# Kernel tuning notes

Measured on AMD Instinct MI355X. Metric: run time of the kernel, lower is better.

Reference implementation:

```python
import jax, jax.numpy as jnp
import numpy as np

N_NODES = 100000
N_EDGES = 1600000
FEAT = 128
HID = 128
CLS = 4


def setup_inputs() -> dict:
    key = jax.random.key(0)
    ks = jax.random.split(key, 10)
    x = jax.random.normal(ks[0], (N_NODES, FEAT), dtype=jnp.float32)
    edge_index = jax.random.randint(ks[1], (2, N_EDGES), 0, N_NODES, dtype=jnp.int64)
    s1 = 1.0 / np.sqrt(FEAT)
    s2 = 1.0 / np.sqrt(HID)
    s3 = 1.0 / np.sqrt(CLS)
    return {
        "x": x,
        "edge_index": edge_index,
        "W1l": jax.random.uniform(ks[2], (HID, FEAT), jnp.float32, -s1, s1),
        "b1": jax.random.uniform(ks[3], (HID,), jnp.float32, -s1, s1),
        "W1r": jax.random.uniform(ks[4], (HID, FEAT), jnp.float32, -s1, s1),
        "W2l": jax.random.uniform(ks[5], (CLS, HID), jnp.float32, -s2, s2),
        "b2": jax.random.uniform(ks[6], (CLS,), jnp.float32, -s2, s2),
        "W2r": jax.random.uniform(ks[7], (CLS, HID), jnp.float32, -s2, s2),
        "Wlin": jax.random.uniform(ks[8], (2, CLS), jnp.float32, -s3, s3),
        "blin": jax.random.uniform(ks[9], (2,), jnp.float32, -s3, s3),
    }


def _sage_conv(h, src, dst, Wl, bl, Wr, n_nodes):
    # PyG SAGEConv (mean aggr, root_weight=True): lin_l(mean_j h_j) + lin_r(h_i)
    msg = h[src]  # [E, d] irregular gather
    agg = jax.ops.segment_sum(msg, dst, num_segments=n_nodes)  # [N, d]
    deg = jax.ops.segment_sum(jnp.ones((src.shape[0], 1), h.dtype), dst,
                              num_segments=n_nodes)  # [N, 1]
    agg = agg / jnp.maximum(deg, 1.0)
    return agg @ Wl.T + bl + h @ Wr.T


def reference(x, edge_index, W1l, b1, W1r, W2l, b2, W2r, Wlin, blin):
    n = x.shape[0]
    src, dst = edge_index[0], edge_index[1]
    h = jax.nn.relu(_sage_conv(x, src, dst, W1l, b1, W1r, n))
    # dropout is identity in eval mode (training=False)
    h = _sage_conv(h, src, dst, W2l, b2, W2r, n)  # [N, 4]
    return h @ Wlin.T + blin  # [N, 2]
```

## Files before the change

### kernel.cpp

```cpp
#include <hip/hip_runtime.h>

#define NN 100000
#define NE 1600000
#define NBUK 1563
#define EB 8192

typedef __attribute__((ext_vector_type(8))) short v8s;
typedef __attribute__((ext_vector_type(4))) float v4f;

__device__ __forceinline__ unsigned short f2bf(float f) {
  unsigned int u = __float_as_uint(f);
  unsigned int r = (u + 0x7FFFu + ((u >> 16) & 1u)) >> 16;
  return (unsigned short)r;
}
__device__ __forceinline__ float bflo(unsigned int w) { return __uint_as_float(w << 16); }
__device__ __forceinline__ float bfhi(unsigned int w) { return __uint_as_float(w & 0xFFFF0000u); }
__device__ __forceinline__ float bf2f(unsigned short w) {
  return __uint_as_float((unsigned int)w << 16);
}


__global__ void k_zerob(int* __restrict__ hist) {
  int i = blockIdx.x * blockDim.x + threadIdx.x;
  if (i < NBUK) hist[i] = 0;
}

__global__ __launch_bounds__(256) void k_hist(const int* __restrict__ dst,
                                              int* __restrict__ hist) {
  __shared__ int lh[NBUK];
  int t = threadIdx.x;
  for (int i = t; i < NBUK; i += 256) lh[i] = 0;
  __syncthreads();
  int base = blockIdx.x * 4096;
  int lim = min(4096, NE - base);
  for (int j = t; j < lim; j += 256) atomicAdd(&lh[dst[base + j] >> 6], 1);
  __syncthreads();
  for (int i = t; i < NBUK; i += 256) {
    int c = lh[i];
    if (c) atomicAdd(&hist[i], c);
  }
}

__global__ __launch_bounds__(256) void k_scanb(const int* __restrict__ hist,
                                               int* __restrict__ bbase,
                                               int* __restrict__ gcur) {
  __shared__ int wsum[4];
  int t = threadIdx.x, w = t >> 6, l = t & 63;
  int carry = 0;
  for (int c = 0; c < (NBUK + 255) / 256; ++c) {
    int i = c * 256 + t;
    int vv = (i < NBUK) ? hist[i] : 0;
    int inc = vv;
#pragma unroll
    for (int o = 1; o < 64; o <<= 1) {
      int uu = __shfl_up(inc, o, 64);
      if (l >= o) inc += uu;
    }
    if (l == 63) wsum[w] = inc;
    __syncthreads();
    int woff = 0;
    for (int j = 0; j < w; ++j) woff += wsum[j];
    int excl = carry + woff + inc - vv;
    if (i < NBUK) { bbase[i] = excl; gcur[i] = excl; }
    int tot = wsum[0] + wsum[1] + wsum[2] + wsum[3];
    __syncthreads();
    carry += tot;
  }
}

__global__ __launch_bounds__(256) void k_scatter(const int* __restrict__ src,
                                                 const int* __restrict__ dst,
                                                 int* __restrict__ gcur,
                                                 unsigned int* __restrict__ staged) {
  __shared__ int lhist[NBUK];
  __shared__ int lcur[NBUK];
  __shared__ int gclaim[NBUK];
  int t = threadIdx.x;
  int e0 = blockIdx.x * EB;
  int ecnt = min(EB, NE - e0);
  for (int i = t; i < NBUK; i += 256) { lhist[i] = 0; lcur[i] = 0; }
  __syncthreads();
  for (int j = t; j < ecnt; j += 256) atomicAdd(&lhist[dst[e0 + j] >> 6], 1);
  __syncthreads();
  for (int b = t; b < NBUK; b += 256) {
    int c = lhist[b];
    gclaim[b] = c ? atomicAdd(&gcur[b], c) : 0;
  }
  __syncthreads();
  for (int j = t; j < ecnt; j += 256) {
    int s = src[e0 + j], d = dst[e0 + j];
    int b = d >> 6;
    int lp = atomicAdd(&lcur[b], 1);
    staged[gclaim[b] + lp] = ((unsigned int)s << 6) | (unsigned int)(d & 63);
  }
}

__global__ __launch_bounds__(256) void k_sort2(const unsigned int* __restrict__ staged,
                                               const int* __restrict__ bbase,
                                               const int* __restrict__ hist,
                                               int* __restrict__ csr,
                                               int* __restrict__ off,
                                               int* __restrict__ deg) {
  __shared__ int h64[64], c64[64];
  int bkt = blockIdx.x, t = threadIdx.x;
  if (t < 64) h64[t] = 0;
  __syncthreads();
  int st = bbase[bkt], cnt = hist[bkt];
  for (int j = t; j < cnt; j += 256) atomicAdd(&h64[staged[st + j] & 63], 1);
  __syncthreads();
  if (t < 64) {
    int v = h64[t];
    int inc = v;
    for (int o = 1; o < 64; o <<= 1) {
      int uu = __shfl_up(inc, o, 64);
      if (t >= o) inc += uu;
    }
    int excl = inc - v;
    c64[t] = excl;
    int node = bkt * 64 + t;
    if (node < NN) { off[node] = st + excl; deg[node] = v; }
  }
  __syncthreads();
  for (int j = t; j < cnt; j += 256) {
    unsigned pk = staged[st + j];
    int lp = atomicAdd(&c64[pk & 63], 1);
    csr[st + lp] = (int)(pk >> 6);
  }
}

extern __shared__ char smem_dyn[];
__global__ __launch_bounds__(512) void k_gemm1(
    const float* __restrict__ x, const float* __restrict__ W1l,
    const float* __restrict__ W1r,
    unsigned short* __restrict__ u, unsigned short* __restrict__ v) {
  char* wlds = smem_dyn;
  int t = threadIdx.x;
  {
    int rsub = t >> 4, chunk = t & 15;
#pragma unroll
    for (int rd = 0; rd < 8; ++rd) {
      int row = rd * 32 + rsub;
      const float* wsrc = (row < 128) ? (W1l + (size_t)row * 128 + chunk * 8)
                                      : (W1r + (size_t)(row - 128) * 128 + chunk * 8);
      float4 f0 = *(const float4*)wsrc;
      float4 f1 = *(const float4*)(wsrc + 4);
      unsigned d0 = (unsigned)f2bf(f0.x) | ((unsigned)f2bf(f0.y) << 16);
      unsigned d1 = (unsigned)f2bf(f0.z) | ((unsigned)f2bf(f0.w) << 16);
      unsigned d2 = (unsigned)f2bf(f1.x) | ((unsigned)f2bf(f1.y) << 16);
      unsigned d3 = (unsigned)f2bf(f1.z) | ((unsigned)f2bf(f1.w) << 16);
      *(uint4*)(wlds + row * 272 + chunk * 16) = make_uint4(d0, d1, d2, d3);
    }
  }

  int wave = t >> 6, l = t & 63;
  int m0 = blockIdx.x * 128 + wave * 16;
  int lr = l & 15, kq = l >> 4;
  int rowc = min(m0 + lr, NN - 1);

  v8s a[4];
#pragma unroll
  for (int ks = 0; ks < 4; ++ks) {
    const float* xp = x + (size_t)rowc * 128 + ks * 32 + kq * 8;
    float4 f0 = *(const float4*)xp;
    float4 f1 = *(const float4*)(xp + 4);
    v8s tv;
    tv[0] = (short)f2bf(f0.x); tv[1] = (short)f2bf(f0.y);
    tv[2] = (short)f2bf(f0.z); tv[3] = (short)f2bf(f0.w);
    tv[4] = (short)f2bf(f1.x); tv[5] = (short)f2bf(f1.y);
    tv[6] = (short)f2bf(f1.z); tv[7] = (short)f2bf(f1.w);
    a[ks] = tv;
  }

  __syncthreads();

  v4f acc[16];
#pragma unroll
  for (int nt = 0; nt < 16; ++nt) acc[nt] = (v4f){0.f, 0.f, 0.f, 0.f};

#pragma unroll
  for (int nt = 0; nt < 16; ++nt) {
    const char* wrow = wlds + (nt * 16 + lr) * 272;
#pragma unroll
    for (int ks = 0; ks < 4; ++ks) {
      v8s b = *(const v8s*)(wrow + ks * 64 + kq * 16);
      acc[nt] = __builtin_amdgcn_mfma_f32_16x16x32_bf16(b, a[ks], acc[nt], 0, 0, 0);
    }
  }

  if (m0 + lr < NN) {
    size_t rowb = (size_t)(m0 + lr) * 128;
#pragma unroll
    for (int nt = 0; nt < 16; ++nt) {
      unsigned lo = (unsigned)f2bf(acc[nt][0]) | ((unsigned)f2bf(acc[nt][1]) << 16);
      unsigned hi = (unsigned)f2bf(acc[nt][2]) | ((unsigned)f2bf(acc[nt][3]) << 16);
      int col = (nt & 7) * 16 + kq * 4;
      if (nt < 8) *(uint2*)(u + rowb + col) = make_uint2(lo, hi);
      else        *(uint2*)(v + rowb + col) = make_uint2(lo, hi);
    }
  }
}

__global__ __launch_bounds__(256) void k_agg(
    const unsigned short* __restrict__ u, const unsigned short* __restrict__ v,
    const int* __restrict__ csr, const int* __restrict__ off, const int* __restrict__ deg,
    const float* __restrict__ b1,
    const float* __restrict__ W2l, const float* __restrict__ W2r,
    float* __restrict__ p, float* __restrict__ r) {
  int wid = (blockIdx.x * blockDim.x + threadIdx.x) >> 6;
  int l = threadIdx.x & 63;
  if (wid >= NN) return;
  int cnt = deg[wid], st = off[wid];
  int half = l >> 5;
  int dpos = l & 31;
  const char* ubase = (const char*)u + (dpos << 3);

  uint2 vw = *(const uint2*)((const char*)v + ((size_t)wid << 8) + (dpos << 3));
  float4 bb = *(const float4*)(b1 + 4 * dpos);
  const float* Wbase = half ? W2r : W2l;
  float4 wv[4];
#pragma unroll
  for (int o = 0; o < 4; ++o) wv[o] = *(const float4*)(Wbase + o * 128 + 4 * dpos);

  float a0 = 0.f, a1 = 0.f, a2 = 0.f, a3 = 0.f;

#define LOADW(W, S) uint2 W = *(const uint2*)(ubase + ((size_t)((unsigned)(S) << 8)))
#define ACCW(W) { a0 += bflo(W.x); a1 += bfhi(W.x); a2 += bflo(W.y); a3 += bfhi(W.y); }

  for (int base = 0; base < cnt; base += 64) {
    int nloc = min(64, cnt - base);
    int idx = 0;
    if (l < nloc) idx = csr[st + base + l];
    int npair = nloc >> 1;
    int e = 0;
    for (; e + 8 <= npair; e += 8) {
      int s0 = __shfl(idx, 2 * e + half, 64);
      int s1 = __shfl(idx, 2 * (e + 1) + half, 64);
      int s2 = __shfl(idx, 2 * (e + 2) + half, 64);
      int s3 = __shfl(idx, 2 * (e + 3) + half, 64);
      int s4 = __shfl(idx, 2 * (e + 4) + half, 64);
      int s5 = __shfl(idx, 2 * (e + 5) + half, 64);
      int s6 = __shfl(idx, 2 * (e + 6) + half, 64);
      int s7 = __shfl(idx, 2 * (e + 7) + half, 64);
      LOADW(w0, s0);
      LOADW(w1, s1);
      LOADW(w2, s2);
      LOADW(w3, s3);
      LOADW(w4, s4);
      LOADW(w5, s5);
      LOADW(w6, s6);
      LOADW(w7, s7);
      ACCW(w0); ACCW(w1); ACCW(w2); ACCW(w3);
      ACCW(w4); ACCW(w5); ACCW(w6); ACCW(w7);
    }
    for (; e + 4 <= npair; e += 4) {
      int s0 = __shfl(idx, 2 * e + half, 64);
      int s1 = __shfl(idx, 2 * (e + 1) + half, 64);
      int s2 = __shfl(idx, 2 * (e + 2) + half, 64);
      int s3 = __shfl(idx, 2 * (e + 3) + half, 64);
      LOADW(w0, s0);
      LOADW(w1, s1);
      LOADW(w2, s2);
      LOADW(w3, s3);
      ACCW(w0); ACCW(w1); ACCW(w2); ACCW(w3);
    }
    for (; e < npair; ++e) {
      int s = __shfl(idx, 2 * e + half, 64);
      LOADW(w, s);
      ACCW(w);
    }
    if (nloc & 1) {
      int s = __shfl(idx, nloc - 1, 64);
      if (half == 0) {
        LOADW(w, s);
        ACCW(w);
      }
    }
  }
#undef LOADW
#undef ACCW

  a0 += __shfl_xor(a0, 32, 64);
  a1 += __shfl_xor(a1, 32, 64);
  a2 += __shfl_xor(a2, 32, 64);
  a3 += __shfl_xor(a3, 32, 64);

  float inv = 1.f / (float)max(cnt, 1);
  float h0 = fmaxf(fmaf(a0, inv, bflo(vw.x) + bb.x), 0.f);
  float h1 = fmaxf(fmaf(a1, inv, bfhi(vw.x) + bb.y), 0.f);
  float h2 = fmaxf(fmaf(a2, inv, bflo(vw.y) + bb.z), 0.f);
  float h3 = fmaxf(fmaf(a3, inv, bfhi(vw.y) + bb.w), 0.f);

  float t0 = h0 * wv[0].x + h1 * wv[0].y + h2 * wv[0].z + h3 * wv[0].w;
  float t1 = h0 * wv[1].x + h1 * wv[1].y + h2 * wv[1].z + h3 * wv[1].w;
  float t2 = h0 * wv[2].x + h1 * wv[2].y + h2 * wv[2].z + h3 * wv[2].w;
  float t3 = h0 * wv[3].x + h1 * wv[3].y + h2 * wv[3].z + h3 * wv[3].w;
  float v01 = (l & 1) ? t1 : t0;
  float w01 = __shfl_xor((l & 1) ? t0 : t1, 1, 64);
  float r01 = v01 + w01;
  float v23 = (l & 1) ? t3 : t2;
  float w23 = __shfl_xor((l & 1) ? t2 : t3, 1, 64);
  float r23 = v23 + w23;
  float vq = (l & 2) ? r23 : r01;
  float wq = __shfl_xor((l & 2) ? r01 : r23, 2, 64);
  float rr = vq + wq;
  rr += __shfl_xor(rr, 4, 64);
  rr += __shfl_xor(rr, 8, 64);
  rr += __shfl_xor(rr, 16, 64);
  float* outp = half ? r : p;
  if (dpos < 4) outp[(size_t)wid * 4 + dpos] = rr;
}

__global__ __launch_bounds__(256) void k_final(
    const float* __restrict__ p, const float* __restrict__ r,
    const int* __restrict__ csr, const int* __restrict__ off,
    const int* __restrict__ deg,
    const float* __restrict__ b2,
    const float* __restrict__ Wlin, const float* __restrict__ blin,
    float* __restrict__ out) {
  int gid = blockIdx.x * blockDim.x + threadIdx.x;
  int node = gid >> 3;
  int sl = gid & 7;
  if (node >= NN) return;
  int cnt = deg[node], st = off[node];
  int l = threadIdx.x & 63;

  float a0 = 0.f, a1 = 0.f, a2 = 0.f, a3 = 0.f;
  for (int e = sl; e < cnt; e += 8) {
    int s = csr[st + e];
    const float4 pv = *(const float4*)(p + (size_t)s * 4);
    a0 += pv.x; a1 += pv.y; a2 += pv.z; a3 += pv.w;
  }
  float v01 = (l & 1) ? a1 : a0;
  float w01 = __shfl_xor((l & 1) ? a0 : a1, 1, 64);
  float r01 = v01 + w01;
  float v23 = (l & 1) ? a3 : a2;
  float w23 = __shfl_xor((l & 1) ? a2 : a3, 1, 64);
  float r23 = v23 + w23;
  float vq = (l & 2) ? r23 : r01;
  float wq = __shfl_xor((l & 2) ? r01 : r23, 2, 64);
  float rr = vq + wq;
  rr += __shfl_xor(rr, 4, 64);
  int o = sl & 3;
  float inv = 1.f / (float)max(cnt, 1);
  float g = rr * inv + b2[o] + r[(size_t)node * 4 + o];
  float t0 = g * Wlin[o];
  float t1 = g * Wlin[4 + o];
  float vv = (l & 1) ? t1 : t0;
  float ww = __shfl_xor((l & 1) ? t0 : t1, 1, 64);
  float q = vv + ww;
  q += __shfl_xor(q, 2, 64);
  if (sl < 2) out[(size_t)node * 2 + sl] = q + blin[sl];
}


extern "C" void kernel_launch(void* const* d_in, const int* in_sizes, int n_in,
                              void* d_out, int out_size, void* d_ws, size_t ws_size,
                              hipStream_t stream) {
  const float* x    = (const float*)d_in[0];
  const int*   ei   = (const int*)d_in[1];
  const int*   src  = ei;
  const int*   dst  = ei + NE;
  const float* W1l  = (const float*)d_in[2];
  const float* b1   = (const float*)d_in[3];
  const float* W1r  = (const float*)d_in[4];
  const float* W2l  = (const float*)d_in[5];
  const float* b2   = (const float*)d_in[6];
  const float* W2r  = (const float*)d_in[7];
  const float* Wlin = (const float*)d_in[8];
  const float* blin = (const float*)d_in[9];
  float* out = (float*)d_out;

  char* w = (char*)d_ws;
  size_t o = 0;
  auto alloc = [&](size_t bytes) {
    void* pp = (void*)(w + o);
    o = (o + bytes + 255) & ~(size_t)255;
    return pp;
  };
  int* hist  = (int*)alloc(NBUK * 4);
  int* bbase = (int*)alloc(NBUK * 4);
  int* gcur  = (int*)alloc(NBUK * 4);
  unsigned int*  staged = (unsigned int*)alloc((size_t)NE * 4);
  int* csr   = (int*)alloc((size_t)NE * 4);
  int* offs  = (int*)alloc(NN * 4);
  int* deg   = (int*)alloc(NN * 4);
  unsigned short* ubuf  = (unsigned short*)alloc((size_t)NN * 128 * 2);
  unsigned short* vbuf  = (unsigned short*)alloc((size_t)NN * 128 * 2);
  float* pbuf = (float*)alloc((size_t)NN * 4 * 4);
  float* rbuf = (float*)alloc((size_t)NN * 4 * 4);

  const size_t gemm1_lds = 256 * 272;

  hipLaunchKernelGGL(k_zerob, dim3((NBUK + 255) / 256), dim3(256), 0, stream, hist);
  hipLaunchKernelGGL(k_hist,  dim3((NE + 4095) / 4096), dim3(256), 0, stream, dst, hist);
  hipLaunchKernelGGL(k_scanb, dim3(1), dim3(256), 0, stream, hist, bbase, gcur);
  hipLaunchKernelGGL(k_scatter, dim3((NE + EB - 1) / EB), dim3(256), 0, stream,
                     src, dst, gcur, staged);
  hipLaunchKernelGGL(k_sort2, dim3(NBUK), dim3(256), 0, stream,
                     staged, bbase, hist, csr, offs, deg);
  hipLaunchKernelGGL(k_gemm1, dim3((NN + 127) / 128), dim3(512), gemm1_lds, stream,
                     x, W1l, W1r, ubuf, vbuf);
  hipLaunchKernelGGL(k_agg,   dim3((NN * 64 + 255) / 256), dim3(256), 0, stream,
                     ubuf, vbuf, csr, offs, deg, b1, W2l, W2r, pbuf, rbuf);
  hipLaunchKernelGGL(k_final, dim3((NN * 8 + 255) / 256), dim3(256), 0, stream,
                     pbuf, rbuf, csr, offs, deg, b2, Wlin, blin, out);
}
```

Measured before the change: 269.2 us.

## Replace bucketed two-pass CSR sort with global atomic degree count and fill

Drops the bucket histogram, scatter and per-bucket local-sort kernels used to build the CSR. It now counts per-node degree with global atomics, runs a three-kernel exclusive scan, and fills the CSR by atomically claiming slots per destination. This avoids the staged intermediate buffer and its extra pass, but brings heavy global atomic contention and a nondeterministic neighbor order inside each row. The aggregation kernel is also split into two half-node launches.

```diff
diff --git a/kernel.cpp b/kernel.cpp
--- a/kernel.cpp
+++ b/kernel.cpp
@@ -2,8 +2,7 @@
 
 #define NN 100000
 #define NE 1600000
-#define NBUK 1563
-#define EB 8192
+#define NHALF 50000
 
 typedef __attribute__((ext_vector_type(8))) short v8s;
 typedef __attribute__((ext_vector_type(4))) float v4f;
@@ -15,41 +14,42 @@
 }
 __device__ __forceinline__ float bflo(unsigned int w) { return __uint_as_float(w << 16); }
 __device__ __forceinline__ float bfhi(unsigned int w) { return __uint_as_float(w & 0xFFFF0000u); }
-__device__ __forceinline__ float bf2f(unsigned short w) {
-  return __uint_as_float((unsigned int)w << 16);
-}
-
-
-__global__ void k_zerob(int* __restrict__ hist) {
+
+
+__global__ __launch_bounds__(256) void k_deg(const int* __restrict__ dst,
+                                             int* __restrict__ deg) {
   int i = blockIdx.x * blockDim.x + threadIdx.x;
-  if (i < NBUK) hist[i] = 0;
-}
-
-__global__ __launch_bounds__(256) void k_hist(const int* __restrict__ dst,
-                                              int* __restrict__ hist) {
-  __shared__ int lh[NBUK];
-  int t = threadIdx.x;
-  for (int i = t; i < NBUK; i += 256) lh[i] = 0;
+  if (i < NE) atomicAdd(&deg[dst[i]], 1);
+}
+
+__global__ __launch_bounds__(256) void k_scan1(const int* __restrict__ deg,
+                                               int* __restrict__ off,
+                                               int* __restrict__ bsum) {
+  __shared__ int wsum[4];
+  int t = threadIdx.x, w = t >> 6, l = t & 63;
+  int i = blockIdx.x * 256 + t;
+  int vv = (i < NN) ? deg[i] : 0;
+  int inc = vv;
+#pragma unroll
+  for (int o = 1; o < 64; o <<= 1) {
+    int uu = __shfl_up(inc, o, 64);
+    if (l >= o) inc += uu;
+  }
+  if (l == 63) wsum[w] = inc;
   __syncthreads();
-  int base = blockIdx.x * 4096;
-  int lim = min(4096, NE - base);
-  for (int j = t; j < lim; j += 256) atomicAdd(&lh[dst[base + j] >> 6], 1);
-  __syncthreads();
-  for (int i = t; i < NBUK; i += 256) {
-    int c = lh[i];
-    if (c) atomicAdd(&hist[i], c);
-  }
-}
-
-__global__ __launch_bounds__(256) void k_scanb(const int* __restrict__ hist,
-                                               int* __restrict__ bbase,
-                                               int* __restrict__ gcur) {
+  int woff = 0;
+  for (int j = 0; j < w; ++j) woff += wsum[j];
+  if (i < NN) off[i] = woff + inc - vv;
+  if (t == 255) bsum[blockIdx.x] = woff + inc;
+}
+
+__global__ __launch_bounds__(256) void k_scan2(int* __restrict__ bsum, int nb) {
   __shared__ int wsum[4];
   int t = threadIdx.x, w = t >> 6, l = t & 63;
   int carry = 0;
-  for (int c = 0; c < (NBUK + 255) / 256; ++c) {
+  for (int c = 0; c * 256 < nb; ++c) {
     int i = c * 256 + t;
-    int vv = (i < NBUK) ? hist[i] : 0;
+    int vv = (i < nb) ? bsum[i] : 0;
     int inc = vv;
 #pragma unroll
     for (int o = 1; o < 64; o <<= 1) {
@@ -60,71 +60,32 @@
     __syncthreads();
     int woff = 0;
     for (int j = 0; j < w; ++j) woff += wsum[j];
-    int excl = carry + woff + inc - vv;
-    if (i < NBUK) { bbase[i] = excl; gcur[i] = excl; }
+    if (i < nb) bsum[i] = carry + woff + inc - vv;
     int tot = wsum[0] + wsum[1] + wsum[2] + wsum[3];
     __syncthreads();
     carry += tot;
   }
 }
 
-__global__ __launch_bounds__(256) void k_scatter(const int* __restrict__ src,
-                                                 const int* __restrict__ dst,
-                                                 int* __restrict__ gcur,
-                                                 unsigned int* __restrict__ staged) {
-  __shared__ int lhist[NBUK];
-  __shared__ int lcur[NBUK];
-  __shared__ int gclaim[NBUK];
-  int t = threadIdx.x;
-  int e0 = blockIdx.x * EB;
-  int ecnt = min(EB, NE - e0);
-  for (int i = t; i < NBUK; i += 256) { lhist[i] = 0; lcur[i] = 0; }
-  __syncthreads();
-  for (int j = t; j < ecnt; j += 256) atomicAdd(&lhist[dst[e0 + j] >> 6], 1);
-  __syncthreads();
-  for (int b = t; b < NBUK; b += 256) {
-    int c = lhist[b];
-    gclaim[b] = c ? atomicAdd(&gcur[b], c) : 0;
-  }
-  __syncthreads();
-  for (int j = t; j < ecnt; j += 256) {
-    int s = src[e0 + j], d = dst[e0 + j];
-    int b = d >> 6;
-    int lp = atomicAdd(&lcur[b], 1);
-    staged[gclaim[b] + lp] = ((unsigned int)s << 6) | (unsigned int)(d & 63);
-  }
-}
-
-__global__ __launch_bounds__(256) void k_sort2(const unsigned int* __restrict__ staged,
-                                               const int* __restrict__ bbase,
-                                               const int* __restrict__ hist,
-                                               int* __restrict__ csr,
+__global__ __launch_bounds__(256) void k_scan3(const int* __restrict__ bsum,
                                                int* __restrict__ off,
-                                               int* __restrict__ deg) {
-  __shared__ int h64[64], c64[64];
-  int bkt = blockIdx.x, t = threadIdx.x;
-  if (t < 64) h64[t] = 0;
-  __syncthreads();
-  int st = bbase[bkt], cnt = hist[bkt];
-  for (int j = t; j < cnt; j += 256) atomicAdd(&h64[staged[st + j] & 63], 1);
-  __syncthreads();
-  if (t < 64) {
-    int v = h64[t];
-    int inc = v;
-    for (int o = 1; o < 64; o <<= 1) {
-      int uu = __shfl_up(inc, o, 64);
-      if (t >= o) inc += uu;
-    }
-    int excl = inc - v;
-    c64[t] = excl;
-    int node = bkt * 64 + t;
-    if (node < NN) { off[node] = st + excl; deg[node] = v; }
-  }
-  __syncthreads();
-  for (int j = t; j < cnt; j += 256) {
-    unsigned pk = staged[st + j];
-    int lp = atomicAdd(&c64[pk & 63], 1);
-    csr[st + lp] = (int)(pk >> 6);
+                                               int* __restrict__ gcur) {
+  int i = blockIdx.x * 256 + threadIdx.x;
+  if (i < NN) {
+    int o = off[i] + bsum[blockIdx.x];
+    off[i] = o;
+    gcur[i] = o;
+  }
+}
+
+__global__ __launch_bounds__(256) void k_fill(const int* __restrict__ src,
+                                              const int* __restrict__ dst,
+                                              int* __restrict__ gcur,
+                                              int* __restrict__ csr) {
+  int i = blockIdx.x * blockDim.x + threadIdx.x;
+  if (i < NE) {
+    int pos = atomicAdd(&gcur[dst[i]], 1);
+    csr[pos] = src[i];
   }
 }
 
@@ -205,8 +166,8 @@
     const int* __restrict__ csr, const int* __restrict__ off, const int* __restrict__ deg,
     const float* __restrict__ b1,
     const float* __restrict__ W2l, const float* __restrict__ W2r,
-    float* __restrict__ p, float* __restrict__ r) {
-  int wid = (blockIdx.x * blockDim.x + threadIdx.x) >> 6;
+    float* __restrict__ p, float* __restrict__ r, int nbase) {
+  int wid = nbase + ((blockIdx.x * blockDim.x + threadIdx.x) >> 6);
   int l = threadIdx.x & 63;
   if (wid >= NN) return;
   int cnt = deg[wid], st = off[wid];
@@ -377,31 +338,32 @@
     o = (o + bytes + 255) & ~(size_t)255;
     return pp;
   };
-  int* hist  = (int*)alloc(NBUK * 4);
-  int* bbase = (int*)alloc(NBUK * 4);
-  int* gcur  = (int*)alloc(NBUK * 4);
-  unsigned int*  staged = (unsigned int*)alloc((size_t)NE * 4);
+  int* deg   = (int*)alloc(NN * 4);
+  int* offs  = (int*)alloc(NN * 4);
+  int* gcur  = (int*)alloc(NN * 4);
+  int* bsum  = (int*)alloc(512 * 4);
   int* csr   = (int*)alloc((size_t)NE * 4);
-  int* offs  = (int*)alloc(NN * 4);
-  int* deg   = (int*)alloc(NN * 4);
   unsigned short* ubuf  = (unsigned short*)alloc((size_t)NN * 128 * 2);
   unsigned short* vbuf  = (unsigned short*)alloc((size_t)NN * 128 * 2);
   float* pbuf = (float*)alloc((size_t)NN * 4 * 4);
   float* rbuf = (float*)alloc((size_t)NN * 4 * 4);
 
+  const int NB = (NN + 255) / 256;
   const size_t gemm1_lds = 256 * 272;
 
-  hipLaunchKernelGGL(k_zerob, dim3((NBUK + 255) / 256), dim3(256), 0, stream, hist);
-  hipLaunchKernelGGL(k_hist,  dim3((NE + 4095) / 4096), dim3(256), 0, stream, dst, hist);
-  hipLaunchKernelGGL(k_scanb, dim3(1), dim3(256), 0, stream, hist, bbase, gcur);
-  hipLaunchKernelGGL(k_scatter, dim3((NE + EB - 1) / EB), dim3(256), 0, stream,
-                     src, dst, gcur, staged);
-  hipLaunchKernelGGL(k_sort2, dim3(NBUK), dim3(256), 0, stream,
-                     staged, bbase, hist, csr, offs, deg);
+  hipMemsetAsync(deg, 0, (size_t)NN * 4, stream);
+  hipLaunchKernelGGL(k_deg,   dim3((NE + 255) / 256), dim3(256), 0, stream, dst, deg);
+  hipLaunchKernelGGL(k_scan1, dim3(NB), dim3(256), 0, stream, deg, offs, bsum);
+  hipLaunchKernelGGL(k_scan2, dim3(1), dim3(256), 0, stream, bsum, NB);
+  hipLaunchKernelGGL(k_scan3, dim3(NB), dim3(256), 0, stream, bsum, offs, gcur);
+  hipLaunchKernelGGL(k_fill,  dim3((NE + 255) / 256), dim3(256), 0, stream,
+                     src, dst, gcur, csr);
   hipLaunchKernelGGL(k_gemm1, dim3((NN + 127) / 128), dim3(512), gemm1_lds, stream,
                      x, W1l, W1r, ubuf, vbuf);
-  hipLaunchKernelGGL(k_agg,   dim3((NN * 64 + 255) / 256), dim3(256), 0, stream,
-                     ubuf, vbuf, csr, offs, deg, b1, W2l, W2r, pbuf, rbuf);
+  hipLaunchKernelGGL(k_agg,   dim3(NHALF * 64 / 256), dim3(256), 0, stream,
+                     ubuf, vbuf, csr, offs, deg, b1, W2l, W2r, pbuf, rbuf, 0);
+  hipLaunchKernelGGL(k_agg,   dim3(NHALF * 64 / 256), dim3(256), 0, stream,
+                     ubuf, vbuf, csr, offs, deg, b1, W2l, W2r, pbuf, rbuf, NHALF);
   hipLaunchKernelGGL(k_final, dim3((NN * 8 + 255) / 256), dim3(256), 0, stream,
                      pbuf, rbuf, csr, offs, deg, b2, Wlin, blin, out);
 }
```

New measurement: 404.8 us. 1.5x slower.

## Fuse CSR build kernels into one cooperative kernel with grid syncs

Applied to the files above, without the earlier changes.

Replaces five separate preprocessing launches (zero, histogram, scan, scatter, per-bucket sort) with a single cooperative kernel of 512 blocks that uses grid.sync between phases. The per-block local histogram is kept in LDS and reused for the scatter claim, so dst is no longer re-histogrammed. The aim is to remove kernel launch gaps and one extra pass over dst. In exchange the scan runs on one block while the others wait at a grid barrier, each block handles about 3125 edges and loops over several buckets in the sort phase, and a cooperative launch is required.

```diff
diff --git a/kernel.cpp b/kernel.cpp
--- a/kernel.cpp
+++ b/kernel.cpp
@@ -1,9 +1,13 @@
 #include <hip/hip_runtime.h>
+#include <hip/hip_cooperative_groups.h>
+
+namespace cg = cooperative_groups;
 
 #define NN 100000
 #define NE 1600000
 #define NBUK 1563
-#define EB 8192
+#define PREB 512
+#define EPB (NE / PREB)
 
 typedef __attribute__((ext_vector_type(8))) short v8s;
 typedef __attribute__((ext_vector_type(4))) float v4f;
@@ -15,116 +19,101 @@
 }
 __device__ __forceinline__ float bflo(unsigned int w) { return __uint_as_float(w << 16); }
 __device__ __forceinline__ float bfhi(unsigned int w) { return __uint_as_float(w & 0xFFFF0000u); }
-__device__ __forceinline__ float bf2f(unsigned short w) {
-  return __uint_as_float((unsigned int)w << 16);
-}
-
-
-__global__ void k_zerob(int* __restrict__ hist) {
-  int i = blockIdx.x * blockDim.x + threadIdx.x;
-  if (i < NBUK) hist[i] = 0;
-}
-
-__global__ __launch_bounds__(256) void k_hist(const int* __restrict__ dst,
-                                              int* __restrict__ hist) {
+
+__global__ __launch_bounds__(256) void k_pre(
+    const int* __restrict__ src, const int* __restrict__ dst,
+    int* __restrict__ hist, int* __restrict__ bbase, int* __restrict__ gcur,
+    unsigned int* __restrict__ staged, int* __restrict__ csr,
+    int* __restrict__ off, int* __restrict__ deg) {
+  cg::grid_group grid = cg::this_grid();
   __shared__ int lh[NBUK];
-  int t = threadIdx.x;
-  for (int i = t; i < NBUK; i += 256) lh[i] = 0;
-  __syncthreads();
-  int base = blockIdx.x * 4096;
-  int lim = min(4096, NE - base);
-  for (int j = t; j < lim; j += 256) atomicAdd(&lh[dst[base + j] >> 6], 1);
+  __shared__ int lcur[NBUK];
+  __shared__ int gclaim[NBUK];
+  __shared__ int wsum[4];
+  __shared__ int h64[64], c64[64];
+  int t = threadIdx.x, b = blockIdx.x;
+
+  for (int i = b * 256 + t; i < NBUK; i += PREB * 256) hist[i] = 0;
+  for (int i = t; i < NBUK; i += 256) { lh[i] = 0; lcur[i] = 0; }
+  __threadfence();
+  grid.sync();
+
+  int e0 = b * EPB;
+  int ecnt = min(EPB, NE - e0);
+  for (int j = t; j < ecnt; j += 256) atomicAdd(&lh[dst[e0 + j] >> 6], 1);
   __syncthreads();
   for (int i = t; i < NBUK; i += 256) {
     int c = lh[i];
     if (c) atomicAdd(&hist[i], c);
   }
-}
-
-__global__ __launch_bounds__(256) void k_scanb(const int* __restrict__ hist,
-                                               int* __restrict__ bbase,
-                                               int* __restrict__ gcur) {
-  __shared__ int wsum[4];
-  int t = threadIdx.x, w = t >> 6, l = t & 63;
-  int carry = 0;
-  for (int c = 0; c < (NBUK + 255) / 256; ++c) {
-    int i = c * 256 + t;
-    int vv = (i < NBUK) ? hist[i] : 0;
-    int inc = vv;
-#pragma unroll
-    for (int o = 1; o < 64; o <<= 1) {
-      int uu = __shfl_up(inc, o, 64);
-      if (l >= o) inc += uu;
-    }
-    if (l == 63) wsum[w] = inc;
-    __syncthreads();
-    int woff = 0;
-    for (int j = 0; j < w; ++j) woff += wsum[j];
-    int excl = carry + woff + inc - vv;
-    if (i < NBUK) { bbase[i] = excl; gcur[i] = excl; }
-    int tot = wsum[0] + wsum[1] + wsum[2] + wsum[3];
-    __syncthreads();
-    carry += tot;
-  }
-}
-
-__global__ __launch_bounds__(256) void k_scatter(const int* __restrict__ src,
-                                                 const int* __restrict__ dst,
-                                                 int* __restrict__ gcur,
-                                                 unsigned int* __restrict__ staged) {
-  __shared__ int lhist[NBUK];
-  __shared__ int lcur[NBUK];
-  __shared__ int gclaim[NBUK];
-  int t = threadIdx.x;
-  int e0 = blockIdx.x * EB;
-  int ecnt = min(EB, NE - e0);
-  for (int i = t; i < NBUK; i += 256) { lhist[i] = 0; lcur[i] = 0; }
-  __syncthreads();
-  for (int j = t; j < ecnt; j += 256) atomicAdd(&lhist[dst[e0 + j] >> 6], 1);
-  __syncthreads();
-  for (int b = t; b < NBUK; b += 256) {
-    int c = lhist[b];
-    gclaim[b] = c ? atomicAdd(&gcur[b], c) : 0;
+  __threadfence();
+  grid.sync();
+
+  if (b == 0) {
+    int w = t >> 6, l = t & 63;
+    int carry = 0;
+    for (int c = 0; c * 256 < NBUK; ++c) {
+      int i = c * 256 + t;
+      int vv = (i < NBUK) ? hist[i] : 0;
+      int inc = vv;
+#pragma unroll
+      for (int o = 1; o < 64; o <<= 1) {
+        int uu = __shfl_up(inc, o, 64);
+        if (l >= o) inc += uu;
+      }
+      if (l == 63) wsum[w] = inc;
+      __syncthreads();
+      int woff = 0;
+      for (int j = 0; j < w; ++j) woff += wsum[j];
+      int excl = carry + woff + inc - vv;
+      if (i < NBUK) { bbase[i] = excl; gcur[i] = excl; }
+      int tot = wsum[0] + wsum[1] + wsum[2] + wsum[3];
+      __syncthreads();
+      carry += tot;
+    }
+    __threadfence();
+  }
+  grid.sync();
+
+  for (int bk = t; bk < NBUK; bk += 256) {
+    int c = lh[bk];
+    gclaim[bk] = c ? atomicAdd(&gcur[bk], c) : 0;
   }
   __syncthreads();
   for (int j = t; j < ecnt; j += 256) {
     int s = src[e0 + j], d = dst[e0 + j];
-    int b = d >> 6;
-    int lp = atomicAdd(&lcur[b], 1);
-    staged[gclaim[b] + lp] = ((unsigned int)s << 6) | (unsigned int)(d & 63);
-  }
-}
-
-__global__ __launch_bounds__(256) void k_sort2(const unsigned int* __restrict__ staged,
-                                               const int* __restrict__ bbase,
-                                               const int* __restrict__ hist,
-                                               int* __restrict__ csr,
-                                               int* __restrict__ off,
-                                               int* __restrict__ deg) {
-  __shared__ int h64[64], c64[64];
-  int bkt = blockIdx.x, t = threadIdx.x;
-  if (t < 64) h64[t] = 0;
-  __syncthreads();
-  int st = bbase[bkt], cnt = hist[bkt];
-  for (int j = t; j < cnt; j += 256) atomicAdd(&h64[staged[st + j] & 63], 1);
-  __syncthreads();
-  if (t < 64) {
-    int v = h64[t];
-    int inc = v;
-    for (int o = 1; o < 64; o <<= 1) {
-      int uu = __shfl_up(inc, o, 64);
-      if (t >= o) inc += uu;
-    }
-    int excl = inc - v;
-    c64[t] = excl;
-    int node = bkt * 64 + t;
-    if (node < NN) { off[node] = st + excl; deg[node] = v; }
-  }
-  __syncthreads();
-  for (int j = t; j < cnt; j += 256) {
-    unsigned pk = staged[st + j];
-    int lp = atomicAdd(&c64[pk & 63], 1);
-    csr[st + lp] = (int)(pk >> 6);
+    int bk = d >> 6;
+    int lp = atomicAdd(&lcur[bk], 1);
+    staged[gclaim[bk] + lp] = ((unsigned int)s << 6) | (unsigned int)(d & 63);
+  }
+  __threadfence();
+  grid.sync();
+
+  for (int bkt = b; bkt < NBUK; bkt += PREB) {
+    if (t < 64) h64[t] = 0;
+    __syncthreads();
+    int st = bbase[bkt], cnt = hist[bkt];
+    for (int j = t; j < cnt; j += 256) atomicAdd(&h64[staged[st + j] & 63], 1);
+    __syncthreads();
+    if (t < 64) {
+      int v = h64[t];
+      int inc = v;
+      for (int o = 1; o < 64; o <<= 1) {
+        int uu = __shfl_up(inc, o, 64);
+        if (t >= o) inc += uu;
+      }
+      int excl = inc - v;
+      c64[t] = excl;
+      int node = bkt * 64 + t;
+      if (node < NN) { off[node] = st + excl; deg[node] = v; }
+    }
+    __syncthreads();
+    for (int j = t; j < cnt; j += 256) {
+      unsigned pk = staged[st + j];
+      int lp = atomicAdd(&c64[pk & 63], 1);
+      csr[st + lp] = (int)(pk >> 6);
+    }
+    __syncthreads();
   }
 }
 
@@ -380,7 +369,7 @@
   int* hist  = (int*)alloc(NBUK * 4);
   int* bbase = (int*)alloc(NBUK * 4);
   int* gcur  = (int*)alloc(NBUK * 4);
-  unsigned int*  staged = (unsigned int*)alloc((size_t)NE * 4);
+  unsigned int* staged = (unsigned int*)alloc((size_t)NE * 4);
   int* csr   = (int*)alloc((size_t)NE * 4);
   int* offs  = (int*)alloc(NN * 4);
   int* deg   = (int*)alloc(NN * 4);
@@ -391,13 +380,11 @@
 
   const size_t gemm1_lds = 256 * 272;
 
-  hipLaunchKernelGGL(k_zerob, dim3((NBUK + 255) / 256), dim3(256), 0, stream, hist);
-  hipLaunchKernelGGL(k_hist,  dim3((NE + 4095) / 4096), dim3(256), 0, stream, dst, hist);
-  hipLaunchKernelGGL(k_scanb, dim3(1), dim3(256), 0, stream, hist, bbase, gcur);
-  hipLaunchKernelGGL(k_scatter, dim3((NE + EB - 1) / EB), dim3(256), 0, stream,
-                     src, dst, gcur, staged);
-  hipLaunchKernelGGL(k_sort2, dim3(NBUK), dim3(256), 0, stream,
-                     staged, bbase, hist, csr, offs, deg);
+  void* pre_args[] = {(void*)&src, (void*)&dst, (void*)&hist, (void*)&bbase,
+                      (void*)&gcur, (void*)&staged, (void*)&csr, (void*)&offs,
+                      (void*)&deg};
+  hipLaunchCooperativeKernel((void*)k_pre, dim3(PREB), dim3(256), pre_args, 0, stream);
+
   hipLaunchKernelGGL(k_gemm1, dim3((NN + 127) / 128), dim3(512), gemm1_lds, stream,
                      x, W1l, W1r, ubuf, vbuf);
   hipLaunchKernelGGL(k_agg,   dim3((NN * 64 + 255) / 256), dim3(256), 0, stream,
```

New measurement: 591.2 us. +119.7%, slower.

## Fuse CSR bucket sort with layer-1 GEMM into one interleaved launch

Applied to the files above, without the earlier changes.

Merges the per-bucket counting sort (k_sort2) and the bf16 MFMA GEMM (k_gemm1) into a single kernel whose even blocks sort buckets and odd blocks compute GEMM tiles. The two independent stages can then overlap on the GPU and one launch is saved. The zeroing kernel is also replaced with hipMemsetAsync. The trade-off is that the sort blocks now run with 512 threads and reserve the GEMM's large dynamic LDS, which may lower occupancy for the sort work, and roughly half of the odd blocks exit immediately.

```diff
diff --git a/kernel.cpp b/kernel.cpp
--- a/kernel.cpp
+++ b/kernel.cpp
@@ -4,6 +4,7 @@
 #define NE 1600000
 #define NBUK 1563
 #define EB 8192
+#define NBLK 782
 
 typedef __attribute__((ext_vector_type(8))) short v8s;
 typedef __attribute__((ext_vector_type(4))) float v4f;
@@ -15,15 +16,7 @@
 }
 __device__ __forceinline__ float bflo(unsigned int w) { return __uint_as_float(w << 16); }
 __device__ __forceinline__ float bfhi(unsigned int w) { return __uint_as_float(w & 0xFFFF0000u); }
-__device__ __forceinline__ float bf2f(unsigned short w) {
-  return __uint_as_float((unsigned int)w << 16);
-}
-
-
-__global__ void k_zerob(int* __restrict__ hist) {
-  int i = blockIdx.x * blockDim.x + threadIdx.x;
-  if (i < NBUK) hist[i] = 0;
-}
+
 
 __global__ __launch_bounds__(256) void k_hist(const int* __restrict__ dst,
                                               int* __restrict__ hist) {
@@ -95,46 +88,49 @@
   }
 }
 
-__global__ __launch_bounds__(256) void k_sort2(const unsigned int* __restrict__ staged,
-                                               const int* __restrict__ bbase,
-                                               const int* __restrict__ hist,
-                                               int* __restrict__ csr,
-                                               int* __restrict__ off,
-                                               int* __restrict__ deg) {
-  __shared__ int h64[64], c64[64];
-  int bkt = blockIdx.x, t = threadIdx.x;
-  if (t < 64) h64[t] = 0;
-  __syncthreads();
-  int st = bbase[bkt], cnt = hist[bkt];
-  for (int j = t; j < cnt; j += 256) atomicAdd(&h64[staged[st + j] & 63], 1);
-  __syncthreads();
-  if (t < 64) {
-    int v = h64[t];
-    int inc = v;
-    for (int o = 1; o < 64; o <<= 1) {
-      int uu = __shfl_up(inc, o, 64);
-      if (t >= o) inc += uu;
-    }
-    int excl = inc - v;
-    c64[t] = excl;
-    int node = bkt * 64 + t;
-    if (node < NN) { off[node] = st + excl; deg[node] = v; }
-  }
-  __syncthreads();
-  for (int j = t; j < cnt; j += 256) {
-    unsigned pk = staged[st + j];
-    int lp = atomicAdd(&c64[pk & 63], 1);
-    csr[st + lp] = (int)(pk >> 6);
-  }
-}
-
 extern __shared__ char smem_dyn[];
-__global__ __launch_bounds__(512) void k_gemm1(
+__global__ __launch_bounds__(512) void k_s2g1(
+    const unsigned int* __restrict__ staged, const int* __restrict__ bbase,
+    const int* __restrict__ hist, int* __restrict__ csr,
+    int* __restrict__ off, int* __restrict__ deg,
     const float* __restrict__ x, const float* __restrict__ W1l,
     const float* __restrict__ W1r,
     unsigned short* __restrict__ u, unsigned short* __restrict__ v) {
+  __shared__ int h64[64], c64[64];
+  int b = blockIdx.x;
+  int t = threadIdx.x;
+
+  if ((b & 1) == 0) {
+    int bkt = b >> 1;
+    if (t < 64) h64[t] = 0;
+    __syncthreads();
+    int st = bbase[bkt], cnt = hist[bkt];
+    for (int j = t; j < cnt; j += 512) atomicAdd(&h64[staged[st + j] & 63], 1);
+    __syncthreads();
+    if (t < 64) {
+      int vv = h64[t];
+      int inc = vv;
+      for (int o = 1; o < 64; o <<= 1) {
+        int uu = __shfl_up(inc, o, 64);
+        if (t >= o) inc += uu;
+      }
+      int excl = inc - vv;
+      c64[t] = excl;
+      int node = bkt * 64 + t;
+      if (node < NN) { off[node] = st + excl; deg[node] = vv; }
+    }
+    __syncthreads();
+    for (int j = t; j < cnt; j += 512) {
+      unsigned pk = staged[st + j];
+      int lp = atomicAdd(&c64[pk & 63], 1);
+      csr[st + lp] = (int)(pk >> 6);
+    }
+    return;
+  }
+
+  int mb = b >> 1;
+  if (mb >= NBLK) return;
   char* wlds = smem_dyn;
-  int t = threadIdx.x;
   {
     int rsub = t >> 4, chunk = t & 15;
 #pragma unroll
@@ -153,7 +149,7 @@
   }
 
   int wave = t >> 6, l = t & 63;
-  int m0 = blockIdx.x * 128 + wave * 16;
+  int m0 = mb * 128 + wave * 16;
   int lr = l & 15, kq = l >> 4;
   int rowc = min(m0 + lr, NN - 1);
 
@@ -182,8 +178,8 @@
     const char* wrow = wlds + (nt * 16 + lr) * 272;
 #pragma unroll
     for (int ks = 0; ks < 4; ++ks) {
-      v8s b = *(const v8s*)(wrow + ks * 64 + kq * 16);
-      acc[nt] = __builtin_amdgcn_mfma_f32_16x16x32_bf16(b, a[ks], acc[nt], 0, 0, 0);
+      v8s bb = *(const v8s*)(wrow + ks * 64 + kq * 16);
+      acc[nt] = __builtin_amdgcn_mfma_f32_16x16x32_bf16(bb, a[ks], acc[nt], 0, 0, 0);
     }
   }
 
@@ -380,7 +376,7 @@
   int* hist  = (int*)alloc(NBUK * 4);
   int* bbase = (int*)alloc(NBUK * 4);
   int* gcur  = (int*)alloc(NBUK * 4);
-  unsigned int*  staged = (unsigned int*)alloc((size_t)NE * 4);
+  unsigned int* staged = (unsigned int*)alloc((size_t)NE * 4);
   int* csr   = (int*)alloc((size_t)NE * 4);
   int* offs  = (int*)alloc(NN * 4);
   int* deg   = (int*)alloc(NN * 4);
@@ -391,15 +387,13 @@
 
   const size_t gemm1_lds = 256 * 272;
 
-  hipLaunchKernelGGL(k_zerob, dim3((NBUK + 255) / 256), dim3(256), 0, stream, hist);
+  hipMemsetAsync(hist, 0, NBUK * 4, stream);
   hipLaunchKernelGGL(k_hist,  dim3((NE + 4095) / 4096), dim3(256), 0, stream, dst, hist);
   hipLaunchKernelGGL(k_scanb, dim3(1), dim3(256), 0, stream, hist, bbase, gcur);
   hipLaunchKernelGGL(k_scatter, dim3((NE + EB - 1) / EB), dim3(256), 0, stream,
                      src, dst, gcur, staged);
-  hipLaunchKernelGGL(k_sort2, dim3(NBUK), dim3(256), 0, stream,
-                     staged, bbase, hist, csr, offs, deg);
-  hipLaunchKernelGGL(k_gemm1, dim3((NN + 127) / 128), dim3(512), gemm1_lds, stream,
-                     x, W1l, W1r, ubuf, vbuf);
+  hipLaunchKernelGGL(k_s2g1, dim3(NBUK * 2), dim3(512), gemm1_lds, stream,
+                     staged, bbase, hist, csr, offs, deg, x, W1l, W1r, ubuf, vbuf);
   hipLaunchKernelGGL(k_agg,   dim3((NN * 64 + 255) / 256), dim3(256), 0, stream,
                      ubuf, vbuf, csr, offs, deg, b1, W2l, W2r, pbuf, rbuf);
   hipLaunchKernelGGL(k_final, dim3((NN * 8 + 255) / 256), dim3(256), 0, stream,
```

After: 283.2 us. +5.2%, slower.
